# Performance work log

Measured on AMD Instinct MI355X. Metric: run time of the kernel, lower is better.

Reference implementation:

```python
import jax, jax.numpy as jnp
import numpy as np

N = 4096
ADP_DIM = 10
TOPK = 20
EPS = 1e-6


def setup_inputs() -> dict:
    key = jax.random.key(0)
    k1, k2, k3, k4, k5, k6 = jax.random.split(key, 6)
    sparsity_mask = (jax.random.uniform(k1, (N, N)) < 0.01).astype(jnp.float32)
    weights = jax.random.uniform(k2, (N, N), dtype=jnp.float32)
    base_adj = sparsity_mask * weights
    return {
        "x_hist": jax.random.normal(k3, (16, 12, N, 2), dtype=jnp.float32),
        "event": jax.random.normal(k4, (16, 12, N, 1), dtype=jnp.float32),
        "base_adj": base_adj,
        "nodevec1": jax.random.normal(k5, (N, ADP_DIM), dtype=jnp.float32),
        "nodevec2": jax.random.normal(k6, (ADP_DIM, N), dtype=jnp.float32),
        "alpha_logit": jnp.asarray(0.0, dtype=jnp.float32),  # sigmoid(0) = alpha_init 0.5
    }


def reference(x_hist, event, base_adj, nodevec1, nodevec2, alpha_logit):
    n = base_adj.shape[0]
    dt = base_adj.dtype

    # ---- history adjacency: cosine-ish similarity -> relu -> row softmax ----
    feat = x_hist.mean(axis=(0, 1))                                  # [N, C]
    feat = feat / (jnp.linalg.norm(feat, axis=1, keepdims=True) + EPS)
    A_h = jax.nn.softmax(jax.nn.relu(feat @ feat.T), axis=1)         # [N, N]

    # ---- event adjacency (Eq. 7 distance decay) ----
    sev = event.mean(axis=(0, 1))[:, 0]                              # [N]
    impacted = (sev > 0.0).astype(dt)
    dist_mx = (base_adj > 0).astype(dt)
    eta = jnp.exp(-0.5 * dist_mx)
    A_e_raw = sev[:, None] * eta * base_adj                          # [N, N]
    A_e = jax.nn.softmax(jax.nn.relu(A_e_raw), axis=1)
    A_e = jnp.where(impacted.sum() > 0, A_e, jnp.zeros_like(A_e))

    # ---- base + learnable adaptive adjacency ----
    A_adp = jax.nn.softmax(jax.nn.relu(nodevec1 @ nodevec2), axis=1)
    A_base = base_adj + A_adp

    # ---- dynamic fusion (Eq. 9) ----
    gamma = jax.nn.sigmoid(alpha_logit)
    A_dyn = gamma * A_h + (1.0 - gamma) * A_e
    A_dyn = 0.5 * A_dyn + 0.5 * A_base

    # ---- top-k row sparsification ----
    _, idx = jax.lax.top_k(A_dyn, TOPK)                              # [N, k]
    mask = jnp.zeros_like(A_dyn).at[jnp.arange(n)[:, None], idx].set(1.0)
    A_dyn = A_dyn * mask

    # ---- symmetric normalization D^{-1/2}(A+I)D^{-1/2} (broadcast form of diag matmuls) ----
    A = A_dyn + jnp.eye(n, dtype=dt)
    deg = A.sum(axis=1)
    d_inv_sqrt = (deg + EPS) ** -0.5
    d_inv_sqrt = jnp.where(jnp.isinf(d_inv_sqrt), jnp.zeros_like(d_inv_sqrt), d_inv_sqrt)
    return d_inv_sqrt[:, None] * A * d_inv_sqrt[None, :]
```

## Files before the change

### kernel.cpp

```cpp
#include <hip/hip_runtime.h>
#include <math.h>

#define NN 4096
#define KTOP 20
#define EPSF 1e-6f

__device__ __forceinline__ float block_rsumf(float v, volatile float* red) {
#pragma unroll
  for (int o = 1; o < 64; o <<= 1) v += __shfl_xor(v, o, 64);
  __syncthreads();
  if ((threadIdx.x & 63) == 0) red[threadIdx.x >> 6] = v;
  __syncthreads();
  return red[0] + red[1] + red[2] + red[3];
}

__global__ __launch_bounds__(256) void k_prep_a(const float* __restrict__ xh,
    const float* __restrict__ ev, float* __restrict__ psx,
    float* __restrict__ psy, float* __restrict__ pse) {
  int ic = blockIdx.x & 15, tc = blockIdx.x >> 4;
  int i = ic * 256 + threadIdx.x;
  const float2* xh2 = (const float2*)xh;
  float sx = 0.f, sy = 0.f, se = 0.f;
  for (int bt = tc * 24; bt < tc * 24 + 24; ++bt) {
    float2 v = xh2[(size_t)bt * NN + i];
    sx += v.x; sy += v.y;
    se += ev[(size_t)bt * NN + i];
  }
  psx[tc * NN + i] = sx; psy[tc * NN + i] = sy; pse[tc * NN + i] = se;
}

__global__ void k_prep_b(const float* __restrict__ psx, const float* __restrict__ psy,
    const float* __restrict__ pse, float2* __restrict__ featn,
    float* __restrict__ sev, int* __restrict__ cnt) {
  int i = blockIdx.x * 256 + threadIdx.x;
  float sx = 0.f, sy = 0.f, se = 0.f;
#pragma unroll
  for (int t = 0; t < 8; ++t) {
    sx += psx[t * NN + i]; sy += psy[t * NN + i]; se += pse[t * NN + i];
  }
  sx *= (1.f / 192.f); sy *= (1.f / 192.f); se *= (1.f / 192.f);
  float nrm = sqrtf(sx * sx + sy * sy) + EPSF;
  featn[i] = make_float2(sx / nrm, sy / nrm);
  sev[i] = se;
  unsigned long long m = __ballot(se > 0.f);
  if ((threadIdx.x & 63) == 0) atomicAdd(cnt, (int)__popcll(m));
}

__global__ __launch_bounds__(256) void k_gemm(const float* __restrict__ nv1,
    const float* __restrict__ nv2, float* __restrict__ aexp) {
  int j = blockIdx.x * 256 + threadIdx.x;
  int i0 = blockIdx.y * 64;
  float w[10];
#pragma unroll
  for (int d = 0; d < 10; ++d) w[d] = nv2[d * NN + j];
#pragma unroll 4
  for (int it = 0; it < 64; ++it) {
    int i = i0 + it;
    const float* r = nv1 + (size_t)i * 10;
    float a = r[0] * w[0] + r[1] * w[1] + r[2] * w[2] + r[3] * w[3] + r[4] * w[4] +
              r[5] * w[5] + r[6] * w[6] + r[7] * w[7] + r[8] * w[8] + r[9] * w[9];
    aexp[(size_t)i * NN + j] = __expf(fmaxf(a, 0.f));
  }
}

__device__ void fb_row(int i, const float (&v)[16], int* kidx, float* kval,
                       float* dinv, volatile float* redf, volatile int* redi,
                       int* eq_js, int* eq_cnt, int* slot) {
  const int tid = threadIdx.x;
  const int lane = tid & 63, wv = tid >> 6;
  unsigned cur = 0;
  for (int bit = 30; bit >= 0; --bit) {
    float tf = __uint_as_float(cur | (1u << bit));
    int lc = 0;
#pragma unroll
    for (int c = 0; c < 16; ++c) lc += (v[c] >= tf) ? 1 : 0;
#pragma unroll
    for (int o = 1; o < 64; o <<= 1) lc += __shfl_xor(lc, o, 64);
    __syncthreads();
    if (lane == 0) redi[wv] = lc;
    __syncthreads();
    int tot = redi[0] + redi[1] + redi[2] + redi[3];
    if (tot >= KTOP) cur |= (1u << bit);
  }
  float T = __uint_as_float(cur);
  int lgt = 0;
#pragma unroll
  for (int c = 0; c < 16; ++c) lgt += (v[c] > T) ? 1 : 0;
#pragma unroll
  for (int o = 1; o < 64; o <<= 1) lgt += __shfl_xor(lgt, o, 64);
  __syncthreads();
  if (lane == 0) redi[wv] = lgt;
  if (tid == 0) *eq_cnt = 0;
  __syncthreads();
  int cgt = redi[0] + redi[1] + redi[2] + redi[3];

  float lsum = 0.f;
#pragma unroll
  for (int c = 0; c < 16; ++c) {
    if (v[c] > T) {
      int p = atomicAdd(slot, 1);
      kidx[i * KTOP + p] = c * 256 + tid;
      kval[i * KTOP + p] = v[c];
      lsum += v[c];
    } else if (v[c] == T) {
      int p = atomicAdd(eq_cnt, 1);
      if (p < 64) eq_js[p] = c * 256 + tid;
    }
  }
  __syncthreads();
  int need = KTOP - cgt;
  if (tid == 0) {
    int m = *eq_cnt < 64 ? *eq_cnt : 64;
    for (int s = 0; s < need; ++s) {
      int best = s;
      for (int u = s + 1; u < m; ++u)
        if (eq_js[u] < eq_js[best]) best = u;
      int tmp = eq_js[s]; eq_js[s] = eq_js[best]; eq_js[best] = tmp;
      kidx[i * KTOP + cgt + s] = eq_js[s];
      kval[i * KTOP + cgt + s] = T;
    }
  }
  float tot = block_rsumf(lsum, redf);
  if (tid == 0) dinv[i] = 1.f / sqrtf(tot + (float)need * T + 1.f + EPSF);
}

__global__ __launch_bounds__(256) void k_row(
    const float* __restrict__ base_adj, const float* __restrict__ aexp,
    const float2* __restrict__ featn, const float* __restrict__ sev,
    const float* __restrict__ alpha, const int* __restrict__ cnt,
    int* __restrict__ kidx, float* __restrict__ kval, float* __restrict__ dinv) {
  const int i = blockIdx.x;
  const int tid = threadIdx.x;
  const int lane = tid & 63, wv = tid >> 6;

  __shared__ float maxima[256];
  __shared__ float candV[64];
  __shared__ int candJ[64];
  __shared__ float redf[12];
  __shared__ int redi[4];
  __shared__ int eq_js[64];
  __shared__ int ccnt, wslot, eq_cnt;
  __shared__ float sTT;

  float2 fi = featn[i];
  float esc = sev[i] * 0.6065306597f;
  float gamma = 1.f / (1.f + __expf(-alpha[0]));

  float b[16], ae[16];
  float hs = 0.f, as = 0.f, ed = 0.f;
#pragma unroll
  for (int c = 0; c < 16; ++c) {
    int j = c * 256 + tid;
    float bb = base_adj[(size_t)i * NN + j];
    float av = aexp[(size_t)i * NN + j];
    float2 fj = featn[j];
    b[c] = bb; ae[c] = av;
    hs += __expf(fmaxf(fi.x * fj.x + fi.y * fj.y, 0.f));
    as += av;
    if (esc > 0.f && bb > 0.f) ed += __expf(esc * bb) - 1.f;
  }
#pragma unroll
  for (int o = 1; o < 64; o <<= 1) {
    hs += __shfl_xor(hs, o, 64);
    as += __shfl_xor(as, o, 64);
    ed += __shfl_xor(ed, o, 64);
  }
  if (lane == 0) { redf[wv * 3] = hs; redf[wv * 3 + 1] = as; redf[wv * 3 + 2] = ed; }
  __syncthreads();
  float HS = redf[0] + redf[3] + redf[6] + redf[9];
  float AS = redf[1] + redf[4] + redf[7] + redf[10];
  float ES = 4096.f + redf[2] + redf[5] + redf[8] + redf[11];

  float eflag = (*cnt > 0) ? 1.f : 0.f;
  float wh = 0.5f * gamma / HS;
  float we = 0.5f * (1.f - gamma) * eflag / ES;
  float wa = 0.5f / AS;

  float v[16];
  float m = 0.f;
#pragma unroll
  for (int c = 0; c < 16; ++c) {
    int j = c * 256 + tid;
    float2 fj = featn[j];
    float he = __expf(fmaxf(fi.x * fj.x + fi.y * fj.y, 0.f));
    float val = wh * he + wa * ae[c] + we;
    if (b[c] > 0.f) {
      float add = 0.5f * b[c];
      if (esc > 0.f) add += we * (__expf(esc * b[c]) - 1.f);
      val += add;
    }
    v[c] = val;
    m = fmaxf(m, val);
  }
  maxima[tid] = m;
  if (tid == 0) { ccnt = 0; wslot = 0; }
  __syncthreads();

  if (wv == 0) {
    float x0 = maxima[lane], x1 = maxima[lane + 64];
    float x2 = maxima[lane + 128], x3 = maxima[lane + 192];
    unsigned cur = 0;
    for (int bit = 30; bit >= 19; --bit) {
      float tf = __uint_as_float(cur | (1u << bit));
      int c_ = __popcll(__ballot(x0 >= tf)) + __popcll(__ballot(x1 >= tf)) +
               __popcll(__ballot(x2 >= tf)) + __popcll(__ballot(x3 >= tf));
      if (c_ >= KTOP) cur |= (1u << bit);
    }
    sTT = __uint_as_float(cur);
  }
  __syncthreads();
  float T0 = sTT;

#pragma unroll
  for (int c = 0; c < 16; ++c) {
    if (v[c] >= T0) {
      int p = atomicAdd(&ccnt, 1);
      if (p < 64) { candV[p] = v[c]; candJ[p] = c * 256 + tid; }
    }
  }
  __syncthreads();
  bool fb = (ccnt > 64);

  if (!fb && wv == 0) {
    int n = ccnt;
    float lv = (lane < n) ? candV[lane] : 0.f;
    int lj = (lane < n) ? candJ[lane] : 0x7FFFFFFF;
    unsigned cur = 0;
    for (int bit = 30; bit >= 0; --bit) {
      float tf = __uint_as_float(cur | (1u << bit));
      if (__popcll(__ballot(lv >= tf)) >= KTOP) cur |= (1u << bit);
    }
    float T = __uint_as_float(cur);
    bool gt = lv > T;
    int cgt = __popcll(__ballot(gt));
    if (gt) {
      int p = atomicAdd(&wslot, 1);
      kidx[i * KTOP + p] = lj;
      kval[i * KTOP + p] = lv;
    }
    int need = KTOP - cgt;
    bool eq = (lv == T);
    for (int k = 0; k < need; ++k) {
      int pj = eq ? lj : 0x7FFFFFFF;
#pragma unroll
      for (int o = 1; o < 64; o <<= 1) {
        int q = __shfl_xor(pj, o, 64);
        pj = q < pj ? q : pj;
      }
      if (lane == 0) {
        kidx[i * KTOP + cgt + k] = pj;
        kval[i * KTOP + cgt + k] = T;
      }
      if (lj == pj) eq = false;
    }
    float ds = gt ? lv : 0.f;
#pragma unroll
    for (int o = 1; o < 64; o <<= 1) ds += __shfl_xor(ds, o, 64);
    if (lane == 0) dinv[i] = 1.f / sqrtf(ds + (float)need * T + 1.f + EPSF);
  }

  if (fb) {
    __syncthreads();
    fb_row(i, v, kidx, kval, dinv, redf, redi, eq_js, &eq_cnt, &wslot);
  }
}

__global__ __launch_bounds__(256) void k_scatter(const int* __restrict__ kidx,
    const float* __restrict__ kval, const float* __restrict__ dinv,
    float* __restrict__ out) {
  int t = blockIdx.x * 256 + threadIdx.x;
  int r = t / 21, s = t - r * 21;
  float di = dinv[r];
  if (s < KTOP) {
    int j = kidx[r * KTOP + s];
    float vv = kval[r * KTOP + s];
    if (j == r) vv += 1.f;
    out[(size_t)r * NN + j] = di * vv * dinv[j];
  } else {
    bool present = false;
#pragma unroll
    for (int k = 0; k < KTOP; ++k) present = present || (kidx[r * KTOP + k] == r);
    if (!present) out[(size_t)r * NN + r] = di * di;
  }
}

extern "C" void kernel_launch(void* const* d_in, const int* in_sizes, int n_in,
                              void* d_out, int out_size, void* d_ws, size_t ws_size,
                              hipStream_t stream) {
  const float* xh    = (const float*)d_in[0];
  const float* ev    = (const float*)d_in[1];
  const float* base  = (const float*)d_in[2];
  const float* nv1   = (const float*)d_in[3];
  const float* nv2   = (const float*)d_in[4];
  const float* alpha = (const float*)d_in[5];
  float* out = (float*)d_out;

  char* ws = (char*)d_ws;
  int*    cnt   = (int*)ws;
  float2* featn = (float2*)(ws + 256);
  float*  sev   = (float*)(ws + 33024);
  float*  dinv  = (float*)(ws + 49408);
  int*    kidx  = (int*)(ws + 65792);
  float*  kval  = (float*)(ws + 393472);
  float*  psx   = (float*)(ws + 721152);
  float*  psy   = (float*)(ws + 852224);
  float*  pse   = (float*)(ws + 983296);

  hipMemsetAsync(cnt, 0, 4, stream);
  k_prep_a<<<128, 256, 0, stream>>>(xh, ev, psx, psy, pse);
  k_prep_b<<<16, 256, 0, stream>>>(psx, psy, pse, featn, sev, cnt);
  k_gemm<<<dim3(16, 64), 256, 0, stream>>>(nv1, nv2, out);
  k_row<<<NN, 256, 0, stream>>>(base, out, featn, sev, alpha, cnt, kidx, kval, dinv);
  hipMemsetAsync(out, 0, (size_t)NN * NN * sizeof(float), stream);
  k_scatter<<<336, 256, 0, stream>>>(kidx, kval, dinv, out);
}
```

Measured before the change: 85.64 us.

## Vectorize row loads, widen gemm outputs, and replace memset+scatter with dense row writer

The gemm kernel now computes four adjacent columns per thread with float4 loads and stores, using a quarter as many blocks. The row kernel changes its element-to-thread mapping so each thread owns 16 contiguous columns and reads them with float4 loads; the top-k index encoding is updated to match. The full-matrix memset and sparse scatter are replaced by one kernel that builds each row in shared memory and writes it densely with float4 stores, folding in the identity and normalization. The cnt memset is folded into the first kernel. The contiguous per-thread mapping gives strided (non-coalesced across lanes) access in k_row, which risks worse memory efficiency there.

```diff
diff --git a/kernel.cpp b/kernel.cpp
--- a/kernel.cpp
+++ b/kernel.cpp
@@ -16,7 +16,8 @@
 
 __global__ __launch_bounds__(256) void k_prep_a(const float* __restrict__ xh,
     const float* __restrict__ ev, float* __restrict__ psx,
-    float* __restrict__ psy, float* __restrict__ pse) {
+    float* __restrict__ psy, float* __restrict__ pse, int* __restrict__ cnt) {
+  if (blockIdx.x == 0 && threadIdx.x == 0) *cnt = 0;
   int ic = blockIdx.x & 15, tc = blockIdx.x >> 4;
   int i = ic * 256 + threadIdx.x;
   const float2* xh2 = (const float2*)xh;
@@ -48,18 +49,25 @@
 
 __global__ __launch_bounds__(256) void k_gemm(const float* __restrict__ nv1,
     const float* __restrict__ nv2, float* __restrict__ aexp) {
-  int j = blockIdx.x * 256 + threadIdx.x;
+  int jt = (blockIdx.x * 256 + threadIdx.x) * 4;
   int i0 = blockIdx.y * 64;
-  float w[10];
-#pragma unroll
-  for (int d = 0; d < 10; ++d) w[d] = nv2[d * NN + j];
-#pragma unroll 4
+  float4 w[10];
+#pragma unroll
+  for (int d = 0; d < 10; ++d) w[d] = *(const float4*)&nv2[d * NN + jt];
   for (int it = 0; it < 64; ++it) {
     int i = i0 + it;
     const float* r = nv1 + (size_t)i * 10;
-    float a = r[0] * w[0] + r[1] * w[1] + r[2] * w[2] + r[3] * w[3] + r[4] * w[4] +
-              r[5] * w[5] + r[6] * w[6] + r[7] * w[7] + r[8] * w[8] + r[9] * w[9];
-    aexp[(size_t)i * NN + j] = __expf(fmaxf(a, 0.f));
+    float4 a = make_float4(0.f, 0.f, 0.f, 0.f);
+#pragma unroll
+    for (int d = 0; d < 10; ++d) {
+      float rd = r[d];
+      a.x += rd * w[d].x; a.y += rd * w[d].y;
+      a.z += rd * w[d].z; a.w += rd * w[d].w;
+    }
+    float4 o;
+    o.x = __expf(fmaxf(a.x, 0.f)); o.y = __expf(fmaxf(a.y, 0.f));
+    o.z = __expf(fmaxf(a.z, 0.f)); o.w = __expf(fmaxf(a.w, 0.f));
+    *(float4*)&aexp[(size_t)i * NN + jt] = o;
   }
 }
 
@@ -99,12 +107,12 @@
   for (int c = 0; c < 16; ++c) {
     if (v[c] > T) {
       int p = atomicAdd(slot, 1);
-      kidx[i * KTOP + p] = c * 256 + tid;
+      kidx[i * KTOP + p] = tid * 16 + c;
       kval[i * KTOP + p] = v[c];
       lsum += v[c];
     } else if (v[c] == T) {
       int p = atomicAdd(eq_cnt, 1);
-      if (p < 64) eq_js[p] = c * 256 + tid;
+      if (p < 64) eq_js[p] = tid * 16 + c;
     }
   }
   __syncthreads();
@@ -132,6 +140,7 @@
   const int i = blockIdx.x;
   const int tid = threadIdx.x;
   const int lane = tid & 63, wv = tid >> 6;
+  const int j0 = tid * 16;
 
   __shared__ float maxima[256];
   __shared__ float candV[64];
@@ -146,19 +155,31 @@
   float esc = sev[i] * 0.6065306597f;
   float gamma = 1.f / (1.f + __expf(-alpha[0]));
 
+  const float4* b4 = (const float4*)(base_adj + (size_t)i * NN + j0);
+  const float4* a4 = (const float4*)(aexp + (size_t)i * NN + j0);
+  const float4* f4 = (const float4*)featn;
+
   float b[16], ae[16];
   float hs = 0.f, as = 0.f, ed = 0.f;
 #pragma unroll
-  for (int c = 0; c < 16; ++c) {
-    int j = c * 256 + tid;
-    float bb = base_adj[(size_t)i * NN + j];
-    float av = aexp[(size_t)i * NN + j];
-    float2 fj = featn[j];
-    b[c] = bb; ae[c] = av;
-    hs += __expf(fmaxf(fi.x * fj.x + fi.y * fj.y, 0.f));
-    as += av;
-    if (esc > 0.f && bb > 0.f) ed += __expf(esc * bb) - 1.f;
-  }
+  for (int q = 0; q < 4; ++q) {
+    float4 B = b4[q], A = a4[q];
+    b[q * 4 + 0] = B.x; b[q * 4 + 1] = B.y; b[q * 4 + 2] = B.z; b[q * 4 + 3] = B.w;
+    ae[q * 4 + 0] = A.x; ae[q * 4 + 1] = A.y; ae[q * 4 + 2] = A.z; ae[q * 4 + 3] = A.w;
+    as += A.x + A.y + A.z + A.w;
+  }
+#pragma unroll
+  for (int p = 0; p < 8; ++p) {
+    float4 fp = f4[tid * 8 + p];
+    hs += __expf(fmaxf(fi.x * fp.x + fi.y * fp.y, 0.f)) +
+          __expf(fmaxf(fi.x * fp.z + fi.y * fp.w, 0.f));
+  }
+  if (esc > 0.f) {
+#pragma unroll
+    for (int c = 0; c < 16; ++c)
+      if (b[c] > 0.f) ed += __expf(esc * b[c]) - 1.f;
+  }
+
 #pragma unroll
   for (int o = 1; o < 64; o <<= 1) {
     hs += __shfl_xor(hs, o, 64);
@@ -179,18 +200,25 @@
   float v[16];
   float m = 0.f;
 #pragma unroll
-  for (int c = 0; c < 16; ++c) {
-    int j = c * 256 + tid;
-    float2 fj = featn[j];
-    float he = __expf(fmaxf(fi.x * fj.x + fi.y * fj.y, 0.f));
-    float val = wh * he + wa * ae[c] + we;
-    if (b[c] > 0.f) {
-      float add = 0.5f * b[c];
-      if (esc > 0.f) add += we * (__expf(esc * b[c]) - 1.f);
-      val += add;
-    }
-    v[c] = val;
-    m = fmaxf(m, val);
+  for (int p = 0; p < 8; ++p) {
+    float4 fp = f4[tid * 8 + p];
+    float he0 = __expf(fmaxf(fi.x * fp.x + fi.y * fp.y, 0.f));
+    float he1 = __expf(fmaxf(fi.x * fp.z + fi.y * fp.w, 0.f));
+    int c0 = 2 * p, c1 = 2 * p + 1;
+    float v0 = wh * he0 + wa * ae[c0] + we;
+    float v1 = wh * he1 + wa * ae[c1] + we;
+    if (b[c0] > 0.f) {
+      float add = 0.5f * b[c0];
+      if (esc > 0.f) add += we * (__expf(esc * b[c0]) - 1.f);
+      v0 += add;
+    }
+    if (b[c1] > 0.f) {
+      float add = 0.5f * b[c1];
+      if (esc > 0.f) add += we * (__expf(esc * b[c1]) - 1.f);
+      v1 += add;
+    }
+    v[c0] = v0; v[c1] = v1;
+    m = fmaxf(m, fmaxf(v0, v1));
   }
   maxima[tid] = m;
   if (tid == 0) { ccnt = 0; wslot = 0; }
@@ -215,7 +243,7 @@
   for (int c = 0; c < 16; ++c) {
     if (v[c] >= T0) {
       int p = atomicAdd(&ccnt, 1);
-      if (p < 64) { candV[p] = v[c]; candJ[p] = c * 256 + tid; }
+      if (p < 64) { candV[p] = v[c]; candJ[p] = j0 + c; }
     }
   }
   __syncthreads();
@@ -265,22 +293,36 @@
   }
 }
 
-__global__ __launch_bounds__(256) void k_scatter(const int* __restrict__ kidx,
-    const float* __restrict__ kval, const float* __restrict__ dinv,
-    float* __restrict__ out) {
-  int t = blockIdx.x * 256 + threadIdx.x;
-  int r = t / 21, s = t - r * 21;
-  float di = dinv[r];
-  if (s < KTOP) {
-    int j = kidx[r * KTOP + s];
-    float vv = kval[r * KTOP + s];
-    if (j == r) vv += 1.f;
-    out[(size_t)r * NN + j] = di * vv * dinv[j];
-  } else {
-    bool present = false;
-#pragma unroll
-    for (int k = 0; k < KTOP; ++k) present = present || (kidx[r * KTOP + k] == r);
-    if (!present) out[(size_t)r * NN + r] = di * di;
+__global__ __launch_bounds__(256) void k_write(
+    const int* __restrict__ kidx, const float* __restrict__ kval,
+    const float* __restrict__ dinv, float* __restrict__ out) {
+  const int i = blockIdx.x;
+  const int tid = threadIdx.x;
+  __shared__ float row[NN];
+  float4* r4 = (float4*)row;
+#pragma unroll
+  for (int c = 0; c < 4; ++c) r4[c * 256 + tid] = make_float4(0.f, 0.f, 0.f, 0.f);
+  __syncthreads();
+  if (tid < KTOP) {
+    int j = kidx[i * KTOP + tid];
+    row[j] = kval[i * KTOP + tid];
+  }
+  __syncthreads();
+  float di = dinv[i];
+  const float4* dv4 = (const float4*)dinv;
+  float4* o4 = (float4*)out;
+#pragma unroll
+  for (int c = 0; c < 4; ++c) {
+    int j4 = c * 256 + tid;
+    float4 rv = r4[j4];
+    float4 dv = dv4[j4];
+    int jb = j4 * 4;
+    float4 o;
+    o.x = di * (rv.x + ((jb + 0) == i ? 1.f : 0.f)) * dv.x;
+    o.y = di * (rv.y + ((jb + 1) == i ? 1.f : 0.f)) * dv.y;
+    o.z = di * (rv.z + ((jb + 2) == i ? 1.f : 0.f)) * dv.z;
+    o.w = di * (rv.w + ((jb + 3) == i ? 1.f : 0.f)) * dv.w;
+    o4[(size_t)i * (NN / 4) + j4] = o;
   }
 }
 
@@ -306,11 +348,9 @@
   float*  psy   = (float*)(ws + 852224);
   float*  pse   = (float*)(ws + 983296);
 
-  hipMemsetAsync(cnt, 0, 4, stream);
-  k_prep_a<<<128, 256, 0, stream>>>(xh, ev, psx, psy, pse);
+  k_prep_a<<<128, 256, 0, stream>>>(xh, ev, psx, psy, pse, cnt);
   k_prep_b<<<16, 256, 0, stream>>>(psx, psy, pse, featn, sev, cnt);
-  k_gemm<<<dim3(16, 64), 256, 0, stream>>>(nv1, nv2, out);
+  k_gemm<<<dim3(4, 64), 256, 0, stream>>>(nv1, nv2, out);
   k_row<<<NN, 256, 0, stream>>>(base, out, featn, sev, alpha, cnt, kidx, kval, dinv);
-  hipMemsetAsync(out, 0, (size_t)NN * NN * sizeof(float), stream);
-  k_scatter<<<336, 256, 0, stream>>>(kidx, kval, dinv, out);
-}
+  k_write<<<NN, 256, 0, stream>>>(kidx, kval, dinv, out);
+}
```

Measured after the change: 100.7 us. 17.6% more time.
